# Kernel tuning notes

Measured on AMD Instinct MI355X. Metric: run time of the kernel, lower is better.

## Reference

```python
import jax, jax.numpy as jnp
import numpy as np

PSEUDO3D = True
DO_TUBE = True
DILATION_ITERATIONS = 1

# Neighbor offsets P2..P9 (clockwise from north), as in Zhang-Suen / skimage skeletonize
_OFFS = [(-1, 0), (-1, 1), (0, 1), (1, 1), (1, 0), (1, -1), (0, -1), (-1, -1)]


def _shift(a, dy, dx):
    # out[n, y, x] = a[n, y+dy, x+dx], zero-padded borders (same as skimage's 0-pad)
    N, H, W = a.shape
    p = jnp.pad(a, ((0, 0), (1, 1), (1, 1)))
    return p[:, 1 + dy:1 + dy + H, 1 + dx:1 + dx + W]


def _subiter(img, first):
    # One Zhang-Suen sub-iteration on a stack of 2D slices [N, H, W] (bool)
    P = [_shift(img, dy, dx) for dy, dx in _OFFS]
    B = sum(p.astype(jnp.int32) for p in P)            # nonzero-neighbor count
    seq = P + [P[0]]
    A = sum(((~seq[k]) & seq[k + 1]).astype(jnp.int32) for k in range(8))  # 0->1 transitions
    P2, P3, P4, P5, P6, P7, P8, P9 = P
    if first:
        c = (~(P2 & P4 & P6)) & (~(P4 & P6 & P8))
    else:
        c = (~(P2 & P4 & P8)) & (~(P2 & P6 & P8))
    remove = img & (B >= 2) & (B <= 6) & (A == 1) & c
    return img & ~remove


def _thin_stack(stack):
    # Zhang-Suen thinning of every 2D slice in a [N, H, W] bool stack, run to convergence.
    # All slices are processed in one while_loop; converged slices are fixed points, so
    # extra iterations are no-ops and the result matches per-slice skeletonize.
    def body(state):
        img, _ = state
        new = _subiter(_subiter(img, True), False)
        return new, jnp.any(new != img)

    def cond(state):
        return state[1]

    img, _ = jax.lax.while_loop(cond, body, (stack, jnp.array(True)))
    return img


def _dilate6(v):
    # scipy.ndimage.binary_dilation with the default 6-connected 3D structure, border 0
    D, H, W = v.shape
    p = jnp.pad(v, 1)
    out = v
    for dz, dy, dx in [(1, 0, 0), (-1, 0, 0), (0, 1, 0), (0, -1, 0), (0, 0, 1), (0, 0, -1)]:
        out = out | p[1 + dz:1 + dz + D, 1 + dy:1 + dy + H, 1 + dx:1 + dx + W]
    return out


def setup_inputs() -> dict:
    key = jax.random.key(0)
    gt = jax.random.randint(key, (1, 48, 384, 384), 0, 2).astype(jnp.float32)
    return {"gt_skel": gt}


def reference(gt_skel):
    vol = gt_skel[0]                      # squeeze(axis=0) -> [D, H, W]
    mask = vol == 1.0                     # bool
    skel = _thin_stack(mask)              # per z-slice skeletonize
    if PSEUDO3D:
        # per y-slice: mask[:, y, :] has shape [D, W]
        skel = skel | jnp.transpose(_thin_stack(jnp.transpose(mask, (1, 0, 2))), (1, 0, 2))
        # per x-slice: mask[:, :, x] has shape [D, H]
        skel = skel | jnp.transpose(_thin_stack(jnp.transpose(mask, (2, 0, 1))), (1, 2, 0))
    if DO_TUBE:
        for _ in range(DILATION_ITERATIONS):
            skel = _dilate6(skel)
    skel = skel & mask                    # skel &= gt_skel.astype(bool) (values are 0/1)
    return skel[None].astype(jnp.float32)
```

## Files before the change

kernel.cpp:

```cpp
#include <hip/hip_runtime.h>

typedef unsigned long long u64;

constexpr int D = 48, H = 384, W = 384;
constexpr int WPR = 6;
constexpr int PADW = 8;
constexpr int NVOX = D * H * W;
constexpr int NWVOL = D * H * WPR;
constexpr int MPAD2 = 52;
constexpr int NXY = (D + 2) * PADW;
constexpr int NTILE = D * 36;

constexpr int BAND = 96;
constexpr int HALO = 16;
constexpr int KA = 16;
constexpr int BROWS = BAND + 2 * HALO;
constexpr int NBAND = H / BAND;

__device__ __forceinline__ void fa(u64 a, u64 b, u64 c, u64& s, u64& cy) {
  u64 x = a ^ b;
  s = x ^ c;
  cy = (a & b) | (c & x);
}

__device__ __forceinline__ u64 zs_regs(u64 w00, u64 w01, u64 w02,
                                       u64 w10, u64 w11, u64 w12,
                                       u64 w20, u64 w21, u64 w22, bool first) {
  const u64 P2 = w01;
  const u64 P3 = (w01 >> 1) | (w02 << 63);
  const u64 P4 = (w11 >> 1) | (w12 << 63);
  const u64 P5 = (w21 >> 1) | (w22 << 63);
  const u64 P6 = w21;
  const u64 P7 = (w21 << 1) | (w20 >> 63);
  const u64 P8 = (w11 << 1) | (w10 >> 63);
  const u64 P9 = (w01 << 1) | (w00 >> 63);

  u64 s1, c1, s2, c2, s3, c3, u0, u1, v1, v2;
  fa(P2, P3, P4, s1, c1);
  fa(P5, P6, P7, s2, c2);
  fa(P8, P9, 0ull, s3, c3);
  fa(s1, s2, s3, u0, u1);
  fa(c1, c2, c3, v1, v2);
  u64 b1 = u1 ^ v1, k2 = u1 & v1;
  u64 b2 = v2 ^ k2, b3 = v2 & k2;
  u64 condB = (b1 | b2 | b3) & ~(b3 | (b2 & b1 & u0));

  u64 t0 = ~P2 & P3, t1 = ~P3 & P4, t2 = ~P4 & P5, t3 = ~P5 & P6;
  u64 t4 = ~P6 & P7, t5 = ~P7 & P8, t6 = ~P8 & P9, t7 = ~P9 & P2;
  fa(t0, t1, t2, s1, c1);
  fa(t3, t4, t5, s2, c2);
  fa(t6, t7, 0ull, s3, c3);
  fa(s1, s2, s3, u0, u1);
  fa(c1, c2, c3, v1, v2);
  u64 a1 = u1 ^ v1, j2 = u1 & v1;
  u64 a2 = v2 ^ j2, a3 = v2 & j2;
  u64 condA = u0 & ~(a1 | a2 | a3);

  u64 cc = first ? ((~(P2 & P4 & P6)) & (~(P4 & P6 & P8)))
                 : ((~(P2 & P4 & P8)) & (~(P2 & P6 & P8)));
  return w11 & ~(condB & condA & cc);
}

__device__ __forceinline__ u64 dirty_wave(const u64* __restrict__ U, int mw) {
  const u64 A = U[mw - 1], B = U[mw], C = U[mw + 1], Dw = U[mw + 2];
  const u64 smA = A | (A >> 1 | B << 63) | (A >> 2 | B << 62);
  const u64 smB = B | (B >> 1 | C << 63) | (B >> 2 | C << 62);
  const u64 smC = C | (C >> 1 | Dw << 63) | (C >> 2 | Dw << 62);
  const u64 Dm9 = (smB << 9) | (smA >> 55);
  const u64 Dm1 = (smB << 1) | (smA >> 63);
  const u64 Dp7 = (smB >> 7) | (smC << 57);
  return Dm9 | Dm1 | Dp7;
}

template<int R, bool FIRST, int NTHR>
__device__ __forceinline__ void subpass(const u64* __restrict__ src, u64* __restrict__ dst,
                                        u64* rawW, const u64* rawPrev,
                                        u64* Uw, const u64* Ur,
                                        int* chgflag, int tid) {
  constexpr int NP = (R + 2) * PADW;
  int anych = 0;
  for (int base = 0; base < NP; base += NTHR) {
    const int idx = base + tid;
    int changed = 0;
    if (idx < NP) {
      const int mw = 1 + (idx >> 6);
      const u64 dmask = dirty_wave(Ur, mw);
      if ((dmask >> (idx & 63)) & 1ull) {
        const u64 old = src[idx];
        u64 nw = 0;
        if (old) {
          nw = zs_regs(src[idx - PADW - 1], src[idx - PADW], src[idx - PADW + 1],
                       src[idx - 1], old, src[idx + 1],
                       src[idx + PADW - 1], src[idx + PADW], src[idx + PADW + 1], FIRST);
          changed = (nw != old);
        }
        dst[idx] = nw;
        anych |= changed;
      }
    }
    const u64 bal = __ballot(changed != 0);
    if ((tid & 63) == 0 && idx < NP) {
      const int mw = 1 + (idx >> 6);
      rawW[mw] = bal;
      Uw[mw] = bal | rawPrev[mw];
    }
  }
  if (anych) *chgflag = 1;
}

template<int MW, int NTHR>
__device__ __forceinline__ void init_masks(u64 (*raw)[MPAD2], u64 (*Um)[MPAD2], int tid) {
  for (int t = tid; t < 4 * MPAD2; t += NTHR) {
    const int arr = t / MPAD2, j = t - arr * MPAD2;
    const u64 v = ((arr & 1) && j >= 1 && j <= MW) ? ~0ull : 0ull;
    if (arr < 2) raw[arr][j] = v; else Um[arr - 2][j] = v;
  }
}

template<bool FIRST>
__device__ __forceinline__ void xy_dense(const u64* __restrict__ src, u64* __restrict__ dst,
                                         int* chgflag, int tid) {
  int anych = 0;
  if (tid < NXY) {
    const u64 old = src[tid];
    u64 nw = 0;
    if (old) {
      nw = zs_regs(src[tid - PADW - 1], src[tid - PADW], src[tid - PADW + 1],
                   src[tid - 1], old, src[tid + 1],
                   src[tid + PADW - 1], src[tid + PADW], src[tid + PADW + 1], FIRST);
      anych = (nw != old);
    }
    dst[tid] = nw;
  }
  if (anych) *chgflag = 1;
}

__device__ __forceinline__ void band_body(const u64* __restrict__ maskP,
                                          u64* __restrict__ curZ,
                                          int zi, int band, u64* Abuf, u64* Bbuf,
                                          u64 (*raw)[MPAD2], u64 (*Um)[MPAD2],
                                          int* s_chg) {
  constexpr int NP = (BROWS + 2) * PADW;
  constexpr int MW = (NP + 63) >> 6;
  const int tid = threadIdx.x;
  const int g0 = band * BAND - HALO;

  for (int idx = tid; idx < NP; idx += 512) {
    const int rp = idx >> 3, cp = idx & 7;
    const int g = g0 + rp - 1;
    u64 v = 0;
    if (rp >= 1 && rp <= BROWS && cp >= 1 && cp <= 6 && g >= 0 && g < H)
      v = maskP[(zi * H + g) * WPR + (cp - 1)];
    Abuf[idx] = v;
    Bbuf[idx] = 0;
  }
  init_masks<MW, 512>(raw, Um, tid);
  if (tid == 0) s_chg[0] = 0;
  __syncthreads();

  for (int t = 0; t < KA; t += 2) {
    subpass<BROWS, true, 512 >(Abuf, Bbuf, raw[0], raw[1], Um[0], Um[1], &s_chg[0], tid);
    __syncthreads();
    subpass<BROWS, false, 512>(Bbuf, Abuf, raw[1], raw[0], Um[1], Um[0], &s_chg[0], tid);
    __syncthreads();
  }

  for (int idx = tid; idx < NP; idx += 512) {
    const int rp = idx >> 3, cp = idx & 7;
    if (rp < 1 || rp > BROWS || cp < 1 || cp > 6) continue;
    const int g = g0 + rp - 1;
    if (g < band * BAND || g >= band * BAND + BAND) continue;
    curZ[(zi * H + g) * WPR + (cp - 1)] = Abuf[idx];
  }
}

template<int MODE>
__device__ __forceinline__ void thin_xy(const u64* __restrict__ srcBuf,
                                        u64* __restrict__ dstBuf,
                                        int slice, u64* Abuf, u64* Bbuf,
                                        int* s_chg) {
  const int tid = threadIdx.x;
  constexpr int S = (MODE == 1) ? H : W;

  if (tid < NXY) {
    const int rp = tid >> 3, cp = tid & 7;
    u64 v = 0;
    if (rp >= 1 && rp <= D && cp >= 1 && cp <= 6)
      v = srcBuf[((rp - 1) * S + slice) * WPR + (cp - 1)];
    Abuf[tid] = v;
    Bbuf[tid] = 0;
  }
  if (tid < 2) s_chg[tid] = 0;
  __syncthreads();

  int k = 0;
  while (true) {
    xy_dense<true >(Abuf, Bbuf, &s_chg[k], tid);
    __syncthreads();
    if (tid == 0) s_chg[k ^ 1] = 0;
    xy_dense<false>(Bbuf, Abuf, &s_chg[k], tid);
    __syncthreads();
    if (s_chg[k] == 0) break;
    k ^= 1;
  }

  if (tid < NXY) {
    const int rp = tid >> 3, cp = tid & 7;
    if (rp >= 1 && rp <= D && cp >= 1 && cp <= 6)
      dstBuf[((rp - 1) * S + slice) * WPR + (cp - 1)] = Abuf[tid];
  }
}

__global__ __launch_bounds__(512) void thin_bands_xy(const u64* __restrict__ maskP,
                                                     const u64* __restrict__ maskPX,
                                                     u64* __restrict__ skelY,
                                                     u64* __restrict__ skelX,
                                                     u64* __restrict__ curZ) {
  __shared__ u64 Abuf[(BROWS + 2) * PADW];
  __shared__ u64 Bbuf[(BROWS + 2) * PADW];
  __shared__ u64 raw[2][MPAD2];
  __shared__ u64 Um[2][MPAD2];
  __shared__ int s_chg[2];
  const int b = blockIdx.x;
  if (b < D * NBAND) {
    band_body(maskP, curZ, b >> 2, b & 3, Abuf, Bbuf, raw, Um, s_chg);
  } else if (b < D * NBAND + W) {
    thin_xy<2>(maskPX, skelX, b - D * NBAND, Abuf, Bbuf, s_chg);
  } else {
    thin_xy<1>(maskP, skelY, b - D * NBAND - W, Abuf, Bbuf, s_chg);
  }
}

__global__ __launch_bounds__(1024) void thin_z_finish(const u64* __restrict__ curZ,
                                                      u64* __restrict__ skelZ,
                                                      const u64* __restrict__ skelX,
                                                      u64* __restrict__ skelXT) {
  __shared__ u64 Abuf[(H + 2) * PADW];
  __shared__ u64 Bbuf[(H + 2) * PADW];
  __shared__ u64 raw[2][MPAD2];
  __shared__ u64 Um[2][MPAD2];
  __shared__ int s_chg[2];
  const int b = blockIdx.x;
  const int tid = threadIdx.x;

  if (b < D) {
    constexpr int NP = (H + 2) * PADW;
    constexpr int MW = (NP + 63) >> 6;
    for (int idx = tid; idx < NP; idx += 1024) {
      const int rp = idx >> 3, cp = idx & 7;
      u64 v = 0;
      if (rp >= 1 && rp <= H && cp >= 1 && cp <= 6)
        v = curZ[(b * H + (rp - 1)) * WPR + (cp - 1)];
      Abuf[idx] = v;
      Bbuf[idx] = 0;
    }
    init_masks<MW, 1024>(raw, Um, tid);
    if (tid < 2) s_chg[tid] = 0;
    __syncthreads();

    int k = 0;
    while (true) {
      subpass<H, true, 1024 >(Abuf, Bbuf, raw[0], raw[1], Um[0], Um[1], &s_chg[k], tid);
      __syncthreads();
      if (tid == 0) s_chg[k ^ 1] = 0;
      subpass<H, false, 1024>(Bbuf, Abuf, raw[1], raw[0], Um[1], Um[0], &s_chg[k], tid);
      __syncthreads();
      if (s_chg[k] == 0) break;
      k ^= 1;
    }

    for (int idx = tid; idx < NP; idx += 1024) {
      const int rp = idx >> 3, cp = idx & 7;
      if (rp < 1 || rp > H || cp < 1 || cp > 6) continue;
      skelZ[(b * H + (rp - 1)) * WPR + (cp - 1)] = Abuf[idx];
    }
  } else {
    const int gw = (b - D) * 16 + (tid >> 6);
    if (gw < NTILE) {
      const int lane = tid & 63;
      const int z = gw / 36, rem = gw - z * 36;
      const int yw = rem / 6, xw = rem - yw * 6;
      const int x = xw * 64 + lane;
      const u64 wx = skelX[(z * W + x) * WPR + yw];
      u64 mine = 0;
      #pragma unroll 8
      for (int j = 0; j < 64; ++j) {
        u64 wj = __ballot((wx >> j) & 1ull);
        if (lane == j) mine = wj;
      }
      const int y = yw * 64 + lane;
      skelXT[(z * H + y) * WPR + xw] = mine;
    }
  }
}

__global__ void init_pack(const float* __restrict__ in, u64* __restrict__ maskP) {
  const int lane = threadIdx.x & 63;
  const int gwave = (blockIdx.x * blockDim.x + threadIdx.x) >> 6;
  const int nwaves = (gridDim.x * blockDim.x) >> 6;
  for (int widx = gwave; widx < NWVOL; widx += nwaves) {
    float v = in[(size_t)widx * 64 + lane];
    u64 w = __ballot(v == 1.0f);
    if (lane == 0) maskP[widx] = w;
  }
}

__global__ void transpose_in(const u64* __restrict__ maskP, u64* __restrict__ maskPX) {
  const int gw = (blockIdx.x * blockDim.x + threadIdx.x) >> 6;
  const int lane = threadIdx.x & 63;
  const int z = gw / 36, rem = gw - z * 36;
  const int yw = rem / 6, xw = rem - yw * 6;
  const u64 wp = maskP[(z * H + yw * 64 + lane) * WPR + xw];
  u64 mine = 0;
  #pragma unroll 8
  for (int i = 0; i < 64; ++i) {
    u64 wi = __ballot((wp >> i) & 1ull);
    if (lane == i) mine = wi;
  }
  maskPX[(z * W + xw * 64 + lane) * WPR + yw] = mine;
}

__global__ __launch_bounds__(256) void dilate_expand(const u64* __restrict__ maskP,
                                                     const u64* __restrict__ sZ,
                                                     const u64* __restrict__ sY,
                                                     const u64* __restrict__ sXT,
                                                     float* __restrict__ out) {
  __shared__ u64 rw[64];
  const int tid = threadIdx.x;
  const int wbase = blockIdx.x * 64;
  if (tid < 64) {
    const int wi = wbase + tid;
    const int wc = wi % WPR;
    const int row = wi / WPR;
    const int y = row % H;
    const int z = row / H;
    const u64 S = sZ[wi] | sY[wi] | sXT[wi];
    const u64 L = (wc > 0) ? (sZ[wi - 1] | sY[wi - 1] | sXT[wi - 1]) : 0ull;
    const u64 Rw = (wc < WPR - 1) ? (sZ[wi + 1] | sY[wi + 1] | sXT[wi + 1]) : 0ull;
    u64 d = S | (S << 1) | (L >> 63) | (S >> 1) | (Rw << 63);
    if (y > 0)     d |= sZ[wi - WPR] | sY[wi - WPR] | sXT[wi - WPR];
    if (y < H - 1) d |= sZ[wi + WPR] | sY[wi + WPR] | sXT[wi + WPR];
    if (z > 0)     d |= sZ[wi - H * WPR] | sY[wi - H * WPR] | sXT[wi - H * WPR];
    if (z < D - 1) d |= sZ[wi + H * WPR] | sY[wi + H * WPR] | sXT[wi + H * WPR];
    rw[tid] = d & maskP[wi];
  }
  __syncthreads();
  float4* o4 = reinterpret_cast<float4*>(out + (size_t)wbase * 64);
  #pragma unroll
  for (int k = 0; k < 4; ++k) {
    const int f = tid + 256 * k;
    const u64 bits = rw[f >> 4] >> ((f & 15) * 4);
    float4 o;
    o.x = (float)(bits & 1ull);
    o.y = (float)((bits >> 1) & 1ull);
    o.z = (float)((bits >> 2) & 1ull);
    o.w = (float)((bits >> 3) & 1ull);
    o4[f] = o;
  }
}

extern "C" void kernel_launch(void* const* d_in, const int* in_sizes, int n_in,
                              void* d_out, int out_size, void* d_ws, size_t ws_size,
                              hipStream_t stream) {
  const float* in = (const float*)d_in[0];
  float* out = (float*)d_out;
  u64* wsw = (u64*)d_ws;
  u64* maskP = wsw;
  u64* maskPX = wsw + NWVOL;
  u64* skelZ = wsw + 2 * NWVOL;
  u64* skelY = wsw + 3 * NWVOL;
  u64* skelX = wsw + 4 * NWVOL;
  u64* skelXT = wsw + 5 * NWVOL;
  u64* curZ = wsw + 6 * NWVOL;

  init_pack<<<1728, 256, 0, stream>>>(in, maskP);
  transpose_in<<<(NTILE * 64) / 256, 256, 0, stream>>>(maskP, maskPX);
  thin_bands_xy<<<D * NBAND + W + H, 512, 0, stream>>>(maskP, maskPX, skelY, skelX, curZ);
  thin_z_finish<<<D + (NTILE + 15) / 16, 1024, 0, stream>>>(curZ, skelZ, skelX, skelXT);
  dilate_expand<<<NWVOL / 64, 256, 0, stream>>>(maskP, skelZ, skelY, skelXT, out);
}
```

Measured before the change: 63.97 us.

## Fuse pack and transpose kernels; carry band worklist masks into z-finish

Merges the input bit-packing and the x/y transpose into one kernel that stages each 64-row chunk in LDS, dropping a launch and a global re-read of the packed mask. The band thinning blocks also export their active-region bitmasks (raw/Um) for their interior rows. The per-slice finishing pass seeds its worklist from those masks instead of initialising all-active, so it can skip tiles that already converged. This relies on the band masks correctly covering the halo boundaries, which adds correctness risk at band seams.

```diff
diff --git a/kernel.cpp b/kernel.cpp
--- a/kernel.cpp
+++ b/kernel.cpp
@@ -137,6 +137,8 @@
 
 __device__ __forceinline__ void band_body(const u64* __restrict__ maskP,
                                           u64* __restrict__ curZ,
+                                          u64* __restrict__ expRaw,
+                                          u64* __restrict__ expUm,
                                           int zi, int band, u64* Abuf, u64* Bbuf,
                                           u64 (*raw)[MPAD2], u64 (*Um)[MPAD2],
                                           int* s_chg) {
@@ -171,6 +173,16 @@
     const int g = g0 + rp - 1;
     if (g < band * BAND || g >= band * BAND + BAND) continue;
     curZ[(zi * H + g) * WPR + (cp - 1)] = Abuf[idx];
+  }
+
+  if (tid < 13) {
+    const int bmw = tid + 3;
+    u64 m = ~0ull;
+    if (tid == 0) m = ~0xFFull;
+    else if (tid == 12) m = 0xFFull;
+    const int eb = (zi * NBAND + band) * 16 + tid;
+    expRaw[eb] = raw[1][bmw] & m;
+    expUm[eb]  = Um[1][bmw] & m;
   }
 }
 
@@ -215,7 +227,9 @@
                                                      const u64* __restrict__ maskPX,
                                                      u64* __restrict__ skelY,
                                                      u64* __restrict__ skelX,
-                                                     u64* __restrict__ curZ) {
+                                                     u64* __restrict__ curZ,
+                                                     u64* __restrict__ expRaw,
+                                                     u64* __restrict__ expUm) {
   __shared__ u64 Abuf[(BROWS + 2) * PADW];
   __shared__ u64 Bbuf[(BROWS + 2) * PADW];
   __shared__ u64 raw[2][MPAD2];
@@ -223,7 +237,7 @@
   __shared__ int s_chg[2];
   const int b = blockIdx.x;
   if (b < D * NBAND) {
-    band_body(maskP, curZ, b >> 2, b & 3, Abuf, Bbuf, raw, Um, s_chg);
+    band_body(maskP, curZ, expRaw, expUm, b >> 2, b & 3, Abuf, Bbuf, raw, Um, s_chg);
   } else if (b < D * NBAND + W) {
     thin_xy<2>(maskPX, skelX, b - D * NBAND, Abuf, Bbuf, s_chg);
   } else {
@@ -234,7 +248,9 @@
 __global__ __launch_bounds__(1024) void thin_z_finish(const u64* __restrict__ curZ,
                                                       u64* __restrict__ skelZ,
                                                       const u64* __restrict__ skelX,
-                                                      u64* __restrict__ skelXT) {
+                                                      u64* __restrict__ skelXT,
+                                                      const u64* __restrict__ expRaw,
+                                                      const u64* __restrict__ expUm) {
   __shared__ u64 Abuf[(H + 2) * PADW];
   __shared__ u64 Bbuf[(H + 2) * PADW];
   __shared__ u64 raw[2][MPAD2];
@@ -245,16 +261,31 @@
 
   if (b < D) {
     constexpr int NP = (H + 2) * PADW;
-    constexpr int MW = (NP + 63) >> 6;
     for (int idx = tid; idx < NP; idx += 1024) {
       const int rp = idx >> 3, cp = idx & 7;
       u64 v = 0;
       if (rp >= 1 && rp <= H && cp >= 1 && cp <= 6)
         v = curZ[(b * H + (rp - 1)) * WPR + (cp - 1)];
       Abuf[idx] = v;
-      Bbuf[idx] = 0;
-    }
-    init_masks<MW, 1024>(raw, Um, tid);
+      Bbuf[idx] = v;
+    }
+    if (tid < MPAD2) {
+      const int j = tid, jj = j - 1;
+      u64 r = 0, u = 0;
+      if (jj >= 0 && jj <= 48) {
+        const int bb = jj / 12, off = jj - 12 * bb;
+        if (bb < NBAND) {
+          r = expRaw[(b * NBAND + bb) * 16 + off];
+          u = expUm[(b * NBAND + bb) * 16 + off];
+        }
+        if (off == 0 && jj > 0) {
+          r |= expRaw[(b * NBAND + (jj / 12 - 1)) * 16 + 12];
+          u |= expUm[(b * NBAND + (jj / 12 - 1)) * 16 + 12];
+        }
+      }
+      raw[1][j] = r; Um[1][j] = u;
+      raw[0][j] = 0; Um[0][j] = 0;
+    }
     if (tid < 2) s_chg[tid] = 0;
     __syncthreads();
 
@@ -294,30 +325,31 @@
   }
 }
 
-__global__ void init_pack(const float* __restrict__ in, u64* __restrict__ maskP) {
-  const int lane = threadIdx.x & 63;
-  const int gwave = (blockIdx.x * blockDim.x + threadIdx.x) >> 6;
-  const int nwaves = (gridDim.x * blockDim.x) >> 6;
-  for (int widx = gwave; widx < NWVOL; widx += nwaves) {
-    float v = in[(size_t)widx * 64 + lane];
-    u64 w = __ballot(v == 1.0f);
-    if (lane == 0) maskP[widx] = w;
-  }
-}
-
-__global__ void transpose_in(const u64* __restrict__ maskP, u64* __restrict__ maskPX) {
-  const int gw = (blockIdx.x * blockDim.x + threadIdx.x) >> 6;
-  const int lane = threadIdx.x & 63;
-  const int z = gw / 36, rem = gw - z * 36;
-  const int yw = rem / 6, xw = rem - yw * 6;
-  const u64 wp = maskP[(z * H + yw * 64 + lane) * WPR + xw];
-  u64 mine = 0;
-  #pragma unroll 8
-  for (int i = 0; i < 64; ++i) {
-    u64 wi = __ballot((wp >> i) & 1ull);
-    if (lane == i) mine = wi;
-  }
-  maskPX[(z * W + xw * 64 + lane) * WPR + yw] = mine;
+__global__ __launch_bounds__(256) void init_pack_tr(const float* __restrict__ in,
+                                                    u64* __restrict__ maskP,
+                                                    u64* __restrict__ maskPX) {
+  __shared__ u64 lds[64 * WPR];
+  const int z = blockIdx.x / 6, yc = blockIdx.x % 6;
+  const int lane = threadIdx.x & 63, wave = threadIdx.x >> 6;
+  for (int w = wave; w < 64 * WPR; w += 4) {
+    const int yl = w / WPR, cp = w - yl * WPR;
+    const int y = yc * 64 + yl;
+    const size_t base = ((size_t)(z * H + y) * WPR + cp) * 64;
+    const float v = in[base + lane];
+    const u64 bits = __ballot(v == 1.0f);
+    if (lane == 0) { lds[w] = bits; maskP[(z * H + y) * WPR + cp] = bits; }
+  }
+  __syncthreads();
+  for (int xw = wave; xw < WPR; xw += 4) {
+    const u64 wp = lds[lane * WPR + xw];
+    u64 mine = 0;
+    #pragma unroll 8
+    for (int i = 0; i < 64; ++i) {
+      u64 wi = __ballot((wp >> i) & 1ull);
+      if (lane == i) mine = wi;
+    }
+    maskPX[(z * W + xw * 64 + lane) * WPR + yc] = mine;
+  }
 }
 
 __global__ __launch_bounds__(256) void dilate_expand(const u64* __restrict__ maskP,
@@ -372,10 +404,13 @@
   u64* skelX = wsw + 4 * NWVOL;
   u64* skelXT = wsw + 5 * NWVOL;
   u64* curZ = wsw + 6 * NWVOL;
-
-  init_pack<<<1728, 256, 0, stream>>>(in, maskP);
-  transpose_in<<<(NTILE * 64) / 256, 256, 0, stream>>>(maskP, maskPX);
-  thin_bands_xy<<<D * NBAND + W + H, 512, 0, stream>>>(maskP, maskPX, skelY, skelX, curZ);
-  thin_z_finish<<<D + (NTILE + 15) / 16, 1024, 0, stream>>>(curZ, skelZ, skelX, skelXT);
+  u64* expRaw = wsw + 7 * NWVOL;
+  u64* expUm = expRaw + 192 * 16;
+
+  init_pack_tr<<<D * 6, 256, 0, stream>>>(in, maskP, maskPX);
+  thin_bands_xy<<<D * NBAND + W + H, 512, 0, stream>>>(maskP, maskPX, skelY, skelX,
+                                                       curZ, expRaw, expUm);
+  thin_z_finish<<<D + (NTILE + 15) / 16, 1024, 0, stream>>>(curZ, skelZ, skelX, skelXT,
+                                                            expRaw, expUm);
   dilate_expand<<<NWVOL / 64, 256, 0, stream>>>(maskP, skelZ, skelY, skelXT, out);
 }
```

New measurement: 87.30 us. 1.36x slower.
